# Kernel optimization log

Measured on AMD Instinct MI355X. Metric: run time of the kernel, lower is better.

## Reference

```python
import jax, jax.numpy as jnp
import numpy as np

EPS = 1e-12  # undefined global `eps` in the original source; standard tiny epsilon


def setup_inputs() -> dict:
    key = jax.random.key(0)
    k1, k2 = jax.random.split(key)
    B, C = 32768, 1000
    output = jax.random.normal(k1, (B, C), dtype=jnp.float32)
    multilabels = (jax.random.uniform(k2, (B, C)) < 0.05).astype(jnp.float32)
    multilabels = multilabels.at[:, 0].set(1.0)
    return {"output": output, "multilabels": multilabels}


def reference(output, multilabels):
    # Equivalent closed form of: for every nonempty subset g of true labels,
    #   loss(g) = -[ pseudo_y*log(o+eps) + (1-pseudo_y)*log(1-o+eps) ].sum()
    #           = base - sum_{j in g} gain_j,
    # with base = -sum_j log(1-o_j+eps) and gain_j = log(o_j+eps)-log(1-o_j+eps).
    # min over nonempty subsets = base - max nonempty-subset gain
    #   = base - (sum of positive gains over true labels, or the max single
    #      gain among true labels if all gains are negative).
    o = jax.nn.sigmoid(output)                      # [B, C]
    log_p = jnp.log(o + EPS)
    log_np = jnp.log(1.0 - o + EPS)
    base = -jnp.sum(log_np, axis=1)                 # [B]
    gain = log_p - log_np                           # [B, C]
    is_true = multilabels == 1.0                    # [B, C] bool (constant)
    pos = is_true & (gain > 0)
    pos_gain = jnp.sum(jnp.where(pos, gain, 0.0), axis=1)          # [B]
    any_pos = jnp.any(pos, axis=1)                                  # [B]
    best_single = jnp.max(jnp.where(is_true, gain, -jnp.inf), axis=1)  # [B]
    max_gain = jnp.where(any_pos, pos_gain, best_single)
    per_sample = base - max_gain                    # [B]
    return jnp.mean(per_sample)
```

## Files before the change

### kernel.cpp

```cpp
#include <hip/hip_runtime.h>
#include <math.h>


constexpr int B = 32768;
constexpr int C = 1000;
constexpr int THREADS = 256;
constexpr int TAIL = 250 - 192;

typedef float f32x4 __attribute__((ext_vector_type(4)));

__device__ __forceinline__ void elem_update(float x, float m,
                                            float& base, float& pos, float& best) {
    float e  = __expf(-fabsf(x));
    float xp = fmaxf(x, 0.0f);
    base += xp + __logf(1.0f + e);
    pos  += m * xp;
    if (m != 0.0f) best = fmaxf(best, x);
}

__device__ __forceinline__ void vec_update(const f32x4& x, const f32x4& m,
                                           float& base, float& pos, float& best) {
    elem_update(x.x, m.x, base, pos, best);
    elem_update(x.y, m.y, base, pos, best);
    elem_update(x.z, m.z, base, pos, best);
    elem_update(x.w, m.w, base, pos, best);
}

__global__ __launch_bounds__(THREADS)
void row_loss_kernel(const float* __restrict__ X,
                     const float* __restrict__ M,
                     float* __restrict__ partial) {
    const int t    = threadIdx.x;
    const int w    = t >> 6;
    const int lane = t & 63;
    const int row  = blockIdx.x * 4 + w;

    const f32x4* x4 = reinterpret_cast<const f32x4*>(X + (size_t)row * C);
    const f32x4* m4 = reinterpret_cast<const f32x4*>(M + (size_t)row * C);

    f32x4 x0 = __builtin_nontemporal_load(x4 + lane);
    f32x4 x1 = __builtin_nontemporal_load(x4 + lane + 64);
    f32x4 x2 = __builtin_nontemporal_load(x4 + lane + 128);
    f32x4 m0 = __builtin_nontemporal_load(m4 + lane);
    f32x4 m1 = __builtin_nontemporal_load(m4 + lane + 64);
    f32x4 m2 = __builtin_nontemporal_load(m4 + lane + 128);
    f32x4 x3 = {-1e30f, -1e30f, -1e30f, -1e30f};
    f32x4 m3 = {0.f, 0.f, 0.f, 0.f};
    if (lane < TAIL) {
        x3 = __builtin_nontemporal_load(x4 + lane + 192);
        m3 = __builtin_nontemporal_load(m4 + lane + 192);
    }

    float b0 = 0.f, b1 = 0.f, b2 = 0.f, b3 = 0.f;
    float p0 = 0.f, p1 = 0.f, p2 = 0.f, p3 = 0.f;
    float s0 = -INFINITY, s1 = -INFINITY, s2 = -INFINITY, s3 = -INFINITY;

    vec_update(x0, m0, b0, p0, s0);
    vec_update(x1, m1, b1, p1, s1);
    vec_update(x2, m2, b2, p2, s2);
    vec_update(x3, m3, b3, p3, s3);

    float base = (b0 + b1) + (b2 + b3);
    float pos  = (p0 + p1) + (p2 + p3);
    float best = fmaxf(fmaxf(s0, s1), fmaxf(s2, s3));

    #pragma unroll
    for (int off = 32; off > 0; off >>= 1) {
        base += __shfl_down(base, off, 64);
        pos  += __shfl_down(pos,  off, 64);
        best  = fmaxf(best, __shfl_down(best, off, 64));
    }

    if (lane == 0)
        partial[row] = base - ((pos > 0.f) ? pos : best);
}

__global__ __launch_bounds__(256)
void finalize1_kernel(const float* __restrict__ partial, float* __restrict__ mid) {
    const int b = blockIdx.x;
    const int t = threadIdx.x;
    float v = partial[b * 512 + t] + partial[b * 512 + t + 256];

    #pragma unroll
    for (int off = 32; off > 0; off >>= 1)
        v += __shfl_down(v, off, 64);

    __shared__ float s[4];
    const int w    = t >> 6;
    const int lane = t & 63;
    if (lane == 0) s[w] = v;
    __syncthreads();
    if (t == 0) mid[b] = (s[0] + s[1]) + (s[2] + s[3]);
}

__global__ __launch_bounds__(64)
void finalize2_kernel(const float* __restrict__ mid, float* __restrict__ out) {
    double v = (double)mid[threadIdx.x];
    #pragma unroll
    for (int off = 32; off > 0; off >>= 1)
        v += __shfl_down(v, off, 64);
    if (threadIdx.x == 0) out[0] = (float)(v / (double)B);
}

extern "C" void kernel_launch(void* const* d_in, const int* in_sizes, int n_in,
                              void* d_out, int out_size, void* d_ws, size_t ws_size,
                              hipStream_t stream) {
    const float* X  = (const float*)d_in[0];
    const float* M  = (const float*)d_in[1];
    float* out      = (float*)d_out;
    float* partial  = (float*)d_ws;
    float* mid      = partial + B;

    row_loss_kernel<<<B / 4, THREADS, 0, stream>>>(X, M, partial);
    finalize1_kernel<<<64, 256, 0, stream>>>(partial, mid);
    finalize2_kernel<<<1, 64, 0, stream>>>(mid, out);
}
```

Measured before the change: 247.8 us.

## Make waves persistent over several rows with double-buffered prefetch of next row

The row kernel now launches 1024 blocks, and each wave processes 8 consecutive rows instead of one. Loads for the next row are issued into a second register buffer before the current row is computed, overlapping memory latency with the transcendental math and the shuffle reduction. The cost is higher register use from two row buffers, which may lower occupancy, and fewer waves in flight to hide latency.

```diff
diff --git a/kernel.cpp b/kernel.cpp
--- a/kernel.cpp
+++ b/kernel.cpp
@@ -4,8 +4,11 @@
 
 constexpr int B = 32768;
 constexpr int C = 1000;
+constexpr int BLOCKS = 1024;
 constexpr int THREADS = 256;
-constexpr int TAIL = 250 - 192;
+constexpr int WAVES = BLOCKS * (THREADS / 64);
+constexpr int RPW = B / WAVES;
+constexpr int TAIL = 58;
 
 typedef float f32x4 __attribute__((ext_vector_type(4)));
 
@@ -19,11 +22,11 @@
 }
 
 __device__ __forceinline__ void vec_update(const f32x4& x, const f32x4& m,
-                                           float& base, float& pos, float& best) {
-    elem_update(x.x, m.x, base, pos, best);
-    elem_update(x.y, m.y, base, pos, best);
-    elem_update(x.z, m.z, base, pos, best);
-    elem_update(x.w, m.w, base, pos, best);
+                                           float& b, float& p, float& s) {
+    elem_update(x.x, m.x, b, p, s);
+    elem_update(x.y, m.y, b, p, s);
+    elem_update(x.z, m.z, b, p, s);
+    elem_update(x.w, m.w, b, p, s);
 }
 
 __global__ __launch_bounds__(THREADS)
@@ -33,46 +36,61 @@
     const int t    = threadIdx.x;
     const int w    = t >> 6;
     const int lane = t & 63;
-    const int row  = blockIdx.x * 4 + w;
+    const int gwave = blockIdx.x * (THREADS / 64) + w;
+    const int row0  = gwave * RPW;
 
-    const f32x4* x4 = reinterpret_cast<const f32x4*>(X + (size_t)row * C);
-    const f32x4* m4 = reinterpret_cast<const f32x4*>(M + (size_t)row * C);
+    f32x4 xb[2][4], mb[2][4];
 
-    f32x4 x0 = __builtin_nontemporal_load(x4 + lane);
-    f32x4 x1 = __builtin_nontemporal_load(x4 + lane + 64);
-    f32x4 x2 = __builtin_nontemporal_load(x4 + lane + 128);
-    f32x4 m0 = __builtin_nontemporal_load(m4 + lane);
-    f32x4 m1 = __builtin_nontemporal_load(m4 + lane + 64);
-    f32x4 m2 = __builtin_nontemporal_load(m4 + lane + 128);
-    f32x4 x3 = {-1e30f, -1e30f, -1e30f, -1e30f};
-    f32x4 m3 = {0.f, 0.f, 0.f, 0.f};
-    if (lane < TAIL) {
-        x3 = __builtin_nontemporal_load(x4 + lane + 192);
-        m3 = __builtin_nontemporal_load(m4 + lane + 192);
+#define LOAD_ROW(buf, r)                                                        \
+    {                                                                           \
+        const f32x4* x4 = reinterpret_cast<const f32x4*>(X + (size_t)(r) * C);  \
+        const f32x4* m4 = reinterpret_cast<const f32x4*>(M + (size_t)(r) * C);  \
+        xb[buf][0] = __builtin_nontemporal_load(x4 + lane);                     \
+        xb[buf][1] = __builtin_nontemporal_load(x4 + lane + 64);                \
+        xb[buf][2] = __builtin_nontemporal_load(x4 + lane + 128);               \
+        mb[buf][0] = __builtin_nontemporal_load(m4 + lane);                     \
+        mb[buf][1] = __builtin_nontemporal_load(m4 + lane + 64);                \
+        mb[buf][2] = __builtin_nontemporal_load(m4 + lane + 128);               \
+        if (lane < TAIL) {                                                      \
+            xb[buf][3] = __builtin_nontemporal_load(x4 + lane + 192);           \
+            mb[buf][3] = __builtin_nontemporal_load(m4 + lane + 192);           \
+        } else {                                                                \
+            xb[buf][3] = (f32x4){-1e30f, -1e30f, -1e30f, -1e30f};               \
+            mb[buf][3] = (f32x4){0.f, 0.f, 0.f, 0.f};                           \
+        }                                                                       \
     }
 
-    float b0 = 0.f, b1 = 0.f, b2 = 0.f, b3 = 0.f;
-    float p0 = 0.f, p1 = 0.f, p2 = 0.f, p3 = 0.f;
-    float s0 = -INFINITY, s1 = -INFINITY, s2 = -INFINITY, s3 = -INFINITY;
-
-    vec_update(x0, m0, b0, p0, s0);
-    vec_update(x1, m1, b1, p1, s1);
-    vec_update(x2, m2, b2, p2, s2);
-    vec_update(x3, m3, b3, p3, s3);
-
-    float base = (b0 + b1) + (b2 + b3);
-    float pos  = (p0 + p1) + (p2 + p3);
-    float best = fmaxf(fmaxf(s0, s1), fmaxf(s2, s3));
+    LOAD_ROW(0, row0);
 
     #pragma unroll
-    for (int off = 32; off > 0; off >>= 1) {
-        base += __shfl_down(base, off, 64);
-        pos  += __shfl_down(pos,  off, 64);
-        best  = fmaxf(best, __shfl_down(best, off, 64));
+    for (int i = 0; i < RPW; ++i) {
+        if (i + 1 < RPW) LOAD_ROW((i + 1) & 1, row0 + i + 1);
+        const int bsel = i & 1;
+
+        float b0 = 0.f, b1 = 0.f, b2 = 0.f, b3 = 0.f;
+        float p0 = 0.f, p1 = 0.f, p2 = 0.f, p3 = 0.f;
+        float s0 = -INFINITY, s1 = -INFINITY, s2 = -INFINITY, s3 = -INFINITY;
+
+        vec_update(xb[bsel][0], mb[bsel][0], b0, p0, s0);
+        vec_update(xb[bsel][1], mb[bsel][1], b1, p1, s1);
+        vec_update(xb[bsel][2], mb[bsel][2], b2, p2, s2);
+        vec_update(xb[bsel][3], mb[bsel][3], b3, p3, s3);
+
+        float base = (b0 + b1) + (b2 + b3);
+        float pos  = (p0 + p1) + (p2 + p3);
+        float best = fmaxf(fmaxf(s0, s1), fmaxf(s2, s3));
+
+        #pragma unroll
+        for (int off = 32; off > 0; off >>= 1) {
+            base += __shfl_down(base, off, 64);
+            pos  += __shfl_down(pos,  off, 64);
+            best  = fmaxf(best, __shfl_down(best, off, 64));
+        }
+
+        if (lane == 0)
+            partial[row0 + i] = base - ((pos > 0.f) ? pos : best);
     }
-
-    if (lane == 0)
-        partial[row] = base - ((pos > 0.f) ? pos : best);
+#undef LOAD_ROW
 }
 
 __global__ __launch_bounds__(256)
@@ -111,7 +129,7 @@
     float* partial  = (float*)d_ws;
     float* mid      = partial + B;
 
-    row_loss_kernel<<<B / 4, THREADS, 0, stream>>>(X, M, partial);
+    row_loss_kernel<<<BLOCKS, THREADS, 0, stream>>>(X, M, partial);
     finalize1_kernel<<<64, 256, 0, stream>>>(partial, mid);
     finalize2_kernel<<<1, 64, 0, stream>>>(mid, out);
 }
```

New measurement: 250.1 us. Within noise of the previous version (+0.9%).
